# Optimization experiments

Measured on AMD Instinct MI355X. Metric: run time of the kernel, lower is better.

## Reference

```python
import jax, jax.numpy as jnp
import numpy as np


def setup_inputs() -> dict:
    key = jax.random.key(0)
    kq, kk, kv = jax.random.split(key, 3)
    B, S, D = 32, 2048, 64
    q = jax.random.normal(kq, (B, S, D), dtype=jnp.float32)
    k = jax.random.normal(kk, (B, S, D), dtype=jnp.float32)
    v = jax.random.normal(kv, (B, S, D), dtype=jnp.float32)
    return {"q": q, "k": k, "v": v}


def reference(q, k, v):
    # attention = q @ k^T  -> [B, S, S]; scale=None, attn_mask=None path
    scores = jnp.einsum("bqd,bkd->bqk", q, k)
    attention = jax.nn.softmax(scores, axis=-1)  # softmax over dim=2 (last)
    # dropout p=0.0 -> identity
    context = jnp.einsum("bqk,bkd->bqd", attention, v) + q  # residual add
    return (context, attention)
```

## Files before the change

### kernel.cpp

```cpp
#include <hip/hip_runtime.h>

namespace {

constexpr int kB = 32;
constexpr int kS = 2048;
constexpr int kD = 64;
constexpr int BQ = 128;
constexpr int BK = 64;
constexpr int LW = 72;
constexpr int NT = kS / BK;
constexpr int NP = NT / 2;
constexpr int KSZ = BK * LW;
constexpr float kLog2e = 1.44269504088896340736f;

typedef _Float16 f16x8 __attribute__((ext_vector_type(8)));
typedef _Float16 f16x4 __attribute__((ext_vector_type(4)));
typedef float f32x4 __attribute__((ext_vector_type(4)));

#define MFMA16F(a, b, c) __builtin_amdgcn_mfma_f32_16x16x32_f16(a, b, c, 0, 0, 0)

#define LBAR()                                                  \
    do {                                                        \
        asm volatile("s_waitcnt lgkmcnt(0)" ::: "memory");      \
        __builtin_amdgcn_s_barrier();                           \
        asm volatile("" ::: "memory");                          \
    } while (0)

__global__ __launch_bounds__(512, 4)
void sdpa_kernel(const float* __restrict__ qg, const float* __restrict__ kg,
                 const float* __restrict__ vg, float* __restrict__ out) {
    __shared__ _Float16 smem[4 * KSZ + 8 * 16 * LW];
    _Float16* sP = smem + 4 * KSZ;
    _Float16* sQ = smem;

    const int tid = threadIdx.x;
    const int lane = tid & 63;
    const int g = lane >> 4;
    const int c = lane & 15;
    const int wq = tid >> 6;
    const int wrow0 = wq * 16;

    const int id = blockIdx.x;
    const int lin = (id & 7) * 64 + (id >> 3);
    const int b = lin >> 4;
    const int q0 = (lin & 15) * BQ;

    float* ctx = out;
    float* att = out + (size_t)kB * kS * kD;
    const size_t inb = (size_t)b * kS * kD;
    const float* kbase = kg + inb;

    const int srow = tid >> 4;
    const int scol = (tid & 15) * 4;

    const int vd = lane;
    const int j0v = wq * 8;

    const int ar = lane >> 4;
    const int ac4 = (lane & 15) * 4;

    f32x4 kr[2][2];
    #pragma unroll
    for (int t = 0; t < 2; ++t)
        #pragma unroll
        for (int i = 0; i < 2; ++i)
            kr[t][i] = *reinterpret_cast<const f32x4*>(
                kbase + (size_t)(t * BK + i * 32 + srow) * kD + scol);

    #pragma unroll
    for (int i = 0; i < 4; ++i) {
        const int row = i * 32 + srow;
        f32x4 qv = *reinterpret_cast<const f32x4*>(qg + inb + (size_t)(q0 + row) * kD + scol);
        f16x4 hv;
        #pragma unroll
        for (int e = 0; e < 4; ++e) hv[e] = (_Float16)(qv[e] * kLog2e);
        *reinterpret_cast<f16x4*>(&sQ[row * LW + scol]) = hv;
    }
    LBAR();
    f16x8 aQ0 = *reinterpret_cast<const f16x8*>(&sQ[(wrow0 + c) * LW + 8 * g]);
    f16x8 aQ1 = *reinterpret_cast<const f16x8*>(&sQ[(wrow0 + c) * LW + 32 + 8 * g]);
    LBAR();

    #pragma unroll
    for (int t = 0; t < 2; ++t)
        #pragma unroll
        for (int i = 0; i < 2; ++i) {
            const int row = i * 32 + srow;
            f16x4 hv;
            #pragma unroll
            for (int e = 0; e < 4; ++e) hv[e] = (_Float16)kr[t][i][e];
            *reinterpret_cast<f16x4*>(&smem[t * KSZ + row * LW + scol]) = hv;
        }
    #pragma unroll
    for (int t = 0; t < 2; ++t)
        #pragma unroll
        for (int i = 0; i < 2; ++i)
            kr[t][i] = *reinterpret_cast<const f32x4*>(
                kbase + (size_t)((2 + t) * BK + i * 32 + srow) * kD + scol);
    LBAR();

    f32x4 l4 = {0.f, 0.f, 0.f, 0.f};

    for (int pt = 0; pt < NP; ++pt) {
        const _Float16* bcur = smem + (pt & 1) * 2 * KSZ;
        _Float16* bnxt = smem + ((pt + 1) & 1) * 2 * KSZ;
        if (pt + 1 < NP) {
            #pragma unroll
            for (int t = 0; t < 2; ++t)
                #pragma unroll
                for (int i = 0; i < 2; ++i) {
                    const int row = i * 32 + srow;
                    f16x4 hv;
                    #pragma unroll
                    for (int e = 0; e < 4; ++e) hv[e] = (_Float16)kr[t][i][e];
                    *reinterpret_cast<f16x4*>(&bnxt[t * KSZ + row * LW + scol]) = hv;
                }
        }
        if (pt + 2 < NP) {
            #pragma unroll
            for (int t = 0; t < 2; ++t)
                #pragma unroll
                for (int i = 0; i < 2; ++i)
                    kr[t][i] = *reinterpret_cast<const f32x4*>(
                        kbase + (size_t)(((pt + 2) * 2 + t) * BK + i * 32 + srow) * kD + scol);
        }
        __builtin_amdgcn_s_setprio(1);
        #pragma unroll
        for (int t = 0; t < 2; ++t) {
            const _Float16* sKc = bcur + t * KSZ;
            #pragma unroll
            for (int ct = 0; ct < 4; ++ct) {
                const int jc = 16 * ct + c;
                f16x8 b0 = *reinterpret_cast<const f16x8*>(&sKc[jc * LW + 8 * g]);
                f16x8 b1 = *reinterpret_cast<const f16x8*>(&sKc[jc * LW + 32 + 8 * g]);
                f32x4 s = {0.f, 0.f, 0.f, 0.f};
                s = MFMA16F(b0, aQ0, s);
                s = MFMA16F(b1, aQ1, s);
                #pragma unroll
                for (int r = 0; r < 4; ++r)
                    l4[r] += __builtin_amdgcn_exp2f(s[r]);
            }
        }
        __builtin_amdgcn_s_setprio(0);
        if (pt + 1 < NP) LBAR();
    }
    float l_l = (l4[0] + l4[1]) + (l4[2] + l4[3]);

    f32x4 kr2[2];
    float vr[8];
    #pragma unroll
    for (int i = 0; i < 2; ++i)
        kr2[i] = *reinterpret_cast<const f32x4*>(kbase + (size_t)(i * 32 + srow) * kD + scol);
    #pragma unroll
    for (int e = 0; e < 8; ++e)
        vr[e] = vg[inb + (size_t)(j0v + e) * kD + vd];

    l_l += __shfl_xor(l_l, 16);
    l_l += __shfl_xor(l_l, 32);
    const float dexp = -__builtin_amdgcn_logf(l_l);

    f32x4 accpv[4];
    #pragma unroll
    for (int dt = 0; dt < 4; ++dt) accpv[dt] = {0.f, 0.f, 0.f, 0.f};

    _Float16* myP = sP + wq * 16 * LW;

    LBAR();
    #pragma unroll
    for (int i = 0; i < 2; ++i) {
        const int row = i * 32 + srow;
        f16x4 hv;
        #pragma unroll
        for (int e = 0; e < 4; ++e) hv[e] = (_Float16)kr2[i][e];
        *reinterpret_cast<f16x4*>(&smem[row * LW + scol]) = hv;
    }
    {
        f16x8 vv;
        #pragma unroll
        for (int e = 0; e < 8; ++e) vv[e] = (_Float16)vr[e];
        *reinterpret_cast<f16x8*>(&smem[2 * KSZ + vd * LW + j0v]) = vv;
    }
    #pragma unroll
    for (int i = 0; i < 2; ++i)
        kr2[i] = *reinterpret_cast<const f32x4*>(kbase + (size_t)(BK + i * 32 + srow) * kD + scol);
    #pragma unroll
    for (int e = 0; e < 8; ++e)
        vr[e] = vg[inb + (size_t)(BK + j0v + e) * kD + vd];
    LBAR();

    for (int kt = 0; kt < NT; ++kt) {
        const int j0 = kt * BK;
        const _Float16* sKc = smem + (kt & 1) * KSZ;
        const _Float16* sVc = smem + 2 * KSZ + (kt & 1) * KSZ;
        _Float16* sKn = smem + ((kt + 1) & 1) * KSZ;
        _Float16* sVn = smem + 2 * KSZ + ((kt + 1) & 1) * KSZ;
        if (kt + 1 < NT) {
            #pragma unroll
            for (int i = 0; i < 2; ++i) {
                const int row = i * 32 + srow;
                f16x4 hv;
                #pragma unroll
                for (int e = 0; e < 4; ++e) hv[e] = (_Float16)kr2[i][e];
                *reinterpret_cast<f16x4*>(&sKn[row * LW + scol]) = hv;
            }
            f16x8 vv;
            #pragma unroll
            for (int e = 0; e < 8; ++e) vv[e] = (_Float16)vr[e];
            *reinterpret_cast<f16x8*>(&sVn[vd * LW + j0v]) = vv;
        }
        if (kt + 2 < NT) {
            const int j0n = (kt + 2) * BK;
            #pragma unroll
            for (int i = 0; i < 2; ++i)
                kr2[i] = *reinterpret_cast<const f32x4*>(kbase + (size_t)(j0n + i * 32 + srow) * kD + scol);
            #pragma unroll
            for (int e = 0; e < 8; ++e)
                vr[e] = vg[inb + (size_t)(j0n + j0v + e) * kD + vd];
        }
        __builtin_amdgcn_s_setprio(1);
        #pragma unroll
        for (int ct = 0; ct < 4; ++ct) {
            const int jc = 16 * ct + c;
            f16x8 b0 = *reinterpret_cast<const f16x8*>(&sKc[jc * LW + 8 * g]);
            f16x8 b1 = *reinterpret_cast<const f16x8*>(&sKc[jc * LW + 32 + 8 * g]);
            f32x4 s = {dexp, dexp, dexp, dexp};
            s = MFMA16F(b0, aQ0, s);
            s = MFMA16F(b1, aQ1, s);
            f16x4 pv;
            #pragma unroll
            for (int r = 0; r < 4; ++r)
                pv[r] = (_Float16)__builtin_amdgcn_exp2f(s[r]);
            *reinterpret_cast<f16x4*>(&myP[c * LW + 16 * ct + 4 * g]) = pv;
        }
        f16x8 aP0 = *reinterpret_cast<const f16x8*>(&myP[c * LW + 8 * g]);
        f16x8 aP1 = *reinterpret_cast<const f16x8*>(&myP[c * LW + 32 + 8 * g]);
        #pragma unroll
        for (int dt = 0; dt < 4; ++dt) {
            f16x8 bv0 = *reinterpret_cast<const f16x8*>(&sVc[(16 * dt + c) * LW + 8 * g]);
            f16x8 bv1 = *reinterpret_cast<const f16x8*>(&sVc[(16 * dt + c) * LW + 32 + 8 * g]);
            accpv[dt] = MFMA16F(aP0, bv0, accpv[dt]);
            accpv[dt] = MFMA16F(aP1, bv1, accpv[dt]);
        }
        __builtin_amdgcn_s_setprio(0);
        #pragma unroll
        for (int i = 0; i < 4; ++i) {
            const int row = 4 * i + ar;
            f16x4 pr = *reinterpret_cast<const f16x4*>(&myP[row * LW + ac4]);
            f32x4 o = {(float)pr[0], (float)pr[1], (float)pr[2], (float)pr[3]};
            *reinterpret_cast<f32x4*>(
                att + ((size_t)b * kS + (size_t)(q0 + wrow0 + row)) * kS + j0 + ac4) = o;
        }
        if (kt + 1 < NT) LBAR();
    }

    #pragma unroll
    for (int dt = 0; dt < 4; ++dt) {
        #pragma unroll
        for (int r = 0; r < 4; ++r) {
            const size_t rowg = (size_t)b * kS + (size_t)(q0 + wrow0 + 4 * g + r);
            const int d = 16 * dt + c;
            ctx[rowg * kD + d] = accpv[dt][r] + qg[rowg * kD + d];
        }
    }
}

}

extern "C" void kernel_launch(void* const* d_in, const int* in_sizes, int n_in,
                              void* d_out, int out_size, void* d_ws, size_t ws_size,
                              hipStream_t stream) {
    const float* q = (const float*)d_in[0];
    const float* k = (const float*)d_in[1];
    const float* v = (const float*)d_in[2];
    float* out = (float*)d_out;
    dim3 grid(kB * (kS / BQ));
    dim3 block(512);
    hipLaunchKernelGGL(sdpa_kernel, grid, block, 0, stream, q, k, v, out);
}
```

Measured before the change: 161.2 us.

## Process two query chunks per block, fusing chunk-1 row sums into chunk-0 output pass

Each block now covers 256 query rows split into two 128-row chunks. The softmax denominator for the second chunk is accumulated during the first chunk's output pass, reusing the same K tiles and fragments. This needs three sweeps over K/V per block instead of four, cutting K loads, fp16 conversion and staging per query row. In exchange the grid is halved, launch bounds drop to 2 blocks per SM, and register pressure rises from the extra Q fragments and accumulators, which may reduce latency hiding.

Measured after the change: 191.3 us. 18.6% more time.

```diff
diff --git a/kernel.cpp b/kernel.cpp
--- a/kernel.cpp
+++ b/kernel.cpp
@@ -5,7 +5,8 @@
 constexpr int kB = 32;
 constexpr int kS = 2048;
 constexpr int kD = 64;
-constexpr int BQ = 128;
+constexpr int BQ = 256;
+constexpr int CH = 128;
 constexpr int BK = 64;
 constexpr int LW = 72;
 constexpr int NT = kS / BK;
@@ -26,7 +27,7 @@
         asm volatile("" ::: "memory");                          \
     } while (0)
 
-__global__ __launch_bounds__(512, 4)
+__global__ __launch_bounds__(512, 2)
 void sdpa_kernel(const float* __restrict__ qg, const float* __restrict__ kg,
                  const float* __restrict__ vg, float* __restrict__ out) {
     __shared__ _Float16 smem[4 * KSZ + 8 * 16 * LW];
@@ -41,9 +42,9 @@
     const int wrow0 = wq * 16;
 
     const int id = blockIdx.x;
-    const int lin = (id & 7) * 64 + (id >> 3);
-    const int b = lin >> 4;
-    const int q0 = (lin & 15) * BQ;
+    const int lin = (id & 7) * 32 + (id >> 3);
+    const int b = lin >> 3;
+    const int q0 = (lin & 7) * BQ;
 
     float* ctx = out;
     float* att = out + (size_t)kB * kS * kD;
@@ -68,7 +69,7 @@
                 kbase + (size_t)(t * BK + i * 32 + srow) * kD + scol);
 
     #pragma unroll
-    for (int i = 0; i < 4; ++i) {
+    for (int i = 0; i < 8; ++i) {
         const int row = i * 32 + srow;
         f32x4 qv = *reinterpret_cast<const f32x4*>(qg + inb + (size_t)(q0 + row) * kD + scol);
         f16x4 hv;
@@ -79,6 +80,8 @@
     LBAR();
     f16x8 aQ0 = *reinterpret_cast<const f16x8*>(&sQ[(wrow0 + c) * LW + 8 * g]);
     f16x8 aQ1 = *reinterpret_cast<const f16x8*>(&sQ[(wrow0 + c) * LW + 32 + 8 * g]);
+    f16x8 aQ2 = *reinterpret_cast<const f16x8*>(&sQ[(CH + wrow0 + c) * LW + 8 * g]);
+    f16x8 aQ3 = *reinterpret_cast<const f16x8*>(&sQ[(CH + wrow0 + c) * LW + 32 + 8 * g]);
     LBAR();
 
     #pragma unroll
@@ -144,7 +147,7 @@
         __builtin_amdgcn_s_setprio(0);
         if (pt + 1 < NP) LBAR();
     }
-    float l_l = (l4[0] + l4[1]) + (l4[2] + l4[3]);
+    float l0 = (l4[0] + l4[1]) + (l4[2] + l4[3]);
 
     f32x4 kr2[2];
     float vr[8];
@@ -155,13 +158,14 @@
     for (int e = 0; e < 8; ++e)
         vr[e] = vg[inb + (size_t)(j0v + e) * kD + vd];
 
-    l_l += __shfl_xor(l_l, 16);
-    l_l += __shfl_xor(l_l, 32);
-    const float dexp = -__builtin_amdgcn_logf(l_l);
+    l0 += __shfl_xor(l0, 16);
+    l0 += __shfl_xor(l0, 32);
+    const float dexp0 = -__builtin_amdgcn_logf(l0);
 
     f32x4 accpv[4];
     #pragma unroll
     for (int dt = 0; dt < 4; ++dt) accpv[dt] = {0.f, 0.f, 0.f, 0.f};
+    f32x4 l14 = {0.f, 0.f, 0.f, 0.f};
 
     _Float16* myP = sP + wq * 16 * LW;
 
@@ -223,14 +227,20 @@
             const int jc = 16 * ct + c;
             f16x8 b0 = *reinterpret_cast<const f16x8*>(&sKc[jc * LW + 8 * g]);
             f16x8 b1 = *reinterpret_cast<const f16x8*>(&sKc[jc * LW + 32 + 8 * g]);
-            f32x4 s = {dexp, dexp, dexp, dexp};
-            s = MFMA16F(b0, aQ0, s);
-            s = MFMA16F(b1, aQ1, s);
+            f32x4 s0 = {dexp0, dexp0, dexp0, dexp0};
+            s0 = MFMA16F(b0, aQ0, s0);
+            s0 = MFMA16F(b1, aQ1, s0);
             f16x4 pv;
             #pragma unroll
             for (int r = 0; r < 4; ++r)
-                pv[r] = (_Float16)__builtin_amdgcn_exp2f(s[r]);
+                pv[r] = (_Float16)__builtin_amdgcn_exp2f(s0[r]);
             *reinterpret_cast<f16x4*>(&myP[c * LW + 16 * ct + 4 * g]) = pv;
+            f32x4 s1 = {0.f, 0.f, 0.f, 0.f};
+            s1 = MFMA16F(b0, aQ2, s1);
+            s1 = MFMA16F(b1, aQ3, s1);
+            #pragma unroll
+            for (int r = 0; r < 4; ++r)
+                l14[r] += __builtin_amdgcn_exp2f(s1[r]);
         }
         f16x8 aP0 = *reinterpret_cast<const f16x8*>(&myP[c * LW + 8 * g]);
         f16x8 aP1 = *reinterpret_cast<const f16x8*>(&myP[c * LW + 32 + 8 * g]);
@@ -254,10 +264,123 @@
     }
 
     #pragma unroll
+    for (int i = 0; i < 2; ++i)
+        kr2[i] = *reinterpret_cast<const f32x4*>(kbase + (size_t)(i * 32 + srow) * kD + scol);
+    #pragma unroll
+    for (int e = 0; e < 8; ++e)
+        vr[e] = vg[inb + (size_t)(j0v + e) * kD + vd];
+
+    float l1 = (l14[0] + l14[1]) + (l14[2] + l14[3]);
+    l1 += __shfl_xor(l1, 16);
+    l1 += __shfl_xor(l1, 32);
+    const float dexp1 = -__builtin_amdgcn_logf(l1);
+
+    #pragma unroll
     for (int dt = 0; dt < 4; ++dt) {
         #pragma unroll
         for (int r = 0; r < 4; ++r) {
             const size_t rowg = (size_t)b * kS + (size_t)(q0 + wrow0 + 4 * g + r);
+            const int d = 16 * dt + c;
+            ctx[rowg * kD + d] = accpv[dt][r] + qg[rowg * kD + d];
+        }
+    }
+
+    #pragma unroll
+    for (int dt = 0; dt < 4; ++dt) accpv[dt] = {0.f, 0.f, 0.f, 0.f};
+
+    LBAR();
+    #pragma unroll
+    for (int i = 0; i < 2; ++i) {
+        const int row = i * 32 + srow;
+        f16x4 hv;
+        #pragma unroll
+        for (int e = 0; e < 4; ++e) hv[e] = (_Float16)kr2[i][e];
+        *reinterpret_cast<f16x4*>(&smem[row * LW + scol]) = hv;
+    }
+    {
+        f16x8 vv;
+        #pragma unroll
+        for (int e = 0; e < 8; ++e) vv[e] = (_Float16)vr[e];
+        *reinterpret_cast<f16x8*>(&smem[2 * KSZ + vd * LW + j0v]) = vv;
+    }
+    #pragma unroll
+    for (int i = 0; i < 2; ++i)
+        kr2[i] = *reinterpret_cast<const f32x4*>(kbase + (size_t)(BK + i * 32 + srow) * kD + scol);
+    #pragma unroll
+    for (int e = 0; e < 8; ++e)
+        vr[e] = vg[inb + (size_t)(BK + j0v + e) * kD + vd];
+    LBAR();
+
+    for (int kt = 0; kt < NT; ++kt) {
+        const int j0 = kt * BK;
+        const _Float16* sKc = smem + (kt & 1) * KSZ;
+        const _Float16* sVc = smem + 2 * KSZ + (kt & 1) * KSZ;
+        _Float16* sKn = smem + ((kt + 1) & 1) * KSZ;
+        _Float16* sVn = smem + 2 * KSZ + ((kt + 1) & 1) * KSZ;
+        if (kt + 1 < NT) {
+            #pragma unroll
+            for (int i = 0; i < 2; ++i) {
+                const int row = i * 32 + srow;
+                f16x4 hv;
+                #pragma unroll
+                for (int e = 0; e < 4; ++e) hv[e] = (_Float16)kr2[i][e];
+                *reinterpret_cast<f16x4*>(&sKn[row * LW + scol]) = hv;
+            }
+            f16x8 vv;
+            #pragma unroll
+            for (int e = 0; e < 8; ++e) vv[e] = (_Float16)vr[e];
+            *reinterpret_cast<f16x8*>(&sVn[vd * LW + j0v]) = vv;
+        }
+        if (kt + 2 < NT) {
+            const int j0n = (kt + 2) * BK;
+            #pragma unroll
+            for (int i = 0; i < 2; ++i)
+                kr2[i] = *reinterpret_cast<const f32x4*>(kbase + (size_t)(j0n + i * 32 + srow) * kD + scol);
+            #pragma unroll
+            for (int e = 0; e < 8; ++e)
+                vr[e] = vg[inb + (size_t)(j0n + j0v + e) * kD + vd];
+        }
+        __builtin_amdgcn_s_setprio(1);
+        #pragma unroll
+        for (int ct = 0; ct < 4; ++ct) {
+            const int jc = 16 * ct + c;
+            f16x8 b0 = *reinterpret_cast<const f16x8*>(&sKc[jc * LW + 8 * g]);
+            f16x8 b1 = *reinterpret_cast<const f16x8*>(&sKc[jc * LW + 32 + 8 * g]);
+            f32x4 s = {dexp1, dexp1, dexp1, dexp1};
+            s = MFMA16F(b0, aQ2, s);
+            s = MFMA16F(b1, aQ3, s);
+            f16x4 pv;
+            #pragma unroll
+            for (int r = 0; r < 4; ++r)
+                pv[r] = (_Float16)__builtin_amdgcn_exp2f(s[r]);
+            *reinterpret_cast<f16x4*>(&myP[c * LW + 16 * ct + 4 * g]) = pv;
+        }
+        f16x8 aP0 = *reinterpret_cast<const f16x8*>(&myP[c * LW + 8 * g]);
+        f16x8 aP1 = *reinterpret_cast<const f16x8*>(&myP[c * LW + 32 + 8 * g]);
+        #pragma unroll
+        for (int dt = 0; dt < 4; ++dt) {
+            f16x8 bv0 = *reinterpret_cast<const f16x8*>(&sVc[(16 * dt + c) * LW + 8 * g]);
+            f16x8 bv1 = *reinterpret_cast<const f16x8*>(&sVc[(16 * dt + c) * LW + 32 + 8 * g]);
+            accpv[dt] = MFMA16F(aP0, bv0, accpv[dt]);
+            accpv[dt] = MFMA16F(aP1, bv1, accpv[dt]);
+        }
+        __builtin_amdgcn_s_setprio(0);
+        #pragma unroll
+        for (int i = 0; i < 4; ++i) {
+            const int row = 4 * i + ar;
+            f16x4 pr = *reinterpret_cast<const f16x4*>(&myP[row * LW + ac4]);
+            f32x4 o = {(float)pr[0], (float)pr[1], (float)pr[2], (float)pr[3]};
+            *reinterpret_cast<f32x4*>(
+                att + ((size_t)b * kS + (size_t)(q0 + CH + wrow0 + row)) * kS + j0 + ac4) = o;
+        }
+        if (kt + 1 < NT) LBAR();
+    }
+
+    #pragma unroll
+    for (int dt = 0; dt < 4; ++dt) {
+        #pragma unroll
+        for (int r = 0; r < 4; ++r) {
+            const size_t rowg = (size_t)b * kS + (size_t)(q0 + CH + wrow0 + 4 * g + r);
             const int d = 16 * dt + c;
             ctx[rowg * kD + d] = accpv[dt][r] + qg[rowg * kD + d];
         }
```
